# Kernel optimization log

Hardware: AMD Instinct MI355X
Metric: run time of the kernel (lower is better)

## Reference

```python
import jax, jax.numpy as jnp
import numpy as np

T, H, I, SI, E, K = 1024, 2048, 1408, 5632, 8, 4
NORM_TOPK_PROB = False


def setup_inputs() -> dict:
    key = jax.random.key(0)
    ks = jax.random.split(key, 9)
    s = lambda k, shape, fan: (jax.random.normal(k, shape, jnp.float32) * (fan ** -0.5))
    return {
        "hidden_states": jax.random.normal(ks[0], (T, H), jnp.float32),
        "Wg": s(ks[1], (E, H, I), H),   # per-expert gate_proj
        "Wu": s(ks[2], (E, H, I), H),   # per-expert up_proj
        "Wd": s(ks[3], (E, I, H), I),   # per-expert down_proj
        "Wsg": s(ks[4], (H, SI), H),    # shared expert gate_proj
        "Wsu": s(ks[5], (H, SI), H),    # shared expert up_proj
        "Wsd": s(ks[6], (SI, H), SI),   # shared expert down_proj
        "W_router": s(ks[7], (H, E), H),        # self.gate
        "W_shared_gate": s(ks[8], (H, 1), H),   # self.shared_expert_gate
    }


def reference(hidden_states, Wg, Wu, Wd, Wsg, Wsu, Wsd, W_router, W_shared_gate):
    x = hidden_states  # [T, H]
    # shared expert: silu(x Wg) * (x Wu) then down proj (fused_gate_up + matmul)
    shared = (jax.nn.silu(x @ Wsg) * (x @ Wsu)) @ Wsd          # [T, H]
    shared_gate = jax.nn.sigmoid(x @ W_shared_gate)            # [T, 1]
    # router: softmax in float32, then top-k
    probs = jax.nn.softmax((x @ W_router).astype(jnp.float32), axis=-1)  # [T, E]
    top_v, top_i = jax.lax.top_k(probs, K)                     # [T, K]
    if NORM_TOPK_PROB and K > 1:
        top_v = top_v / jnp.sum(top_v, axis=-1, keepdims=True)
    # combine weights: zero for non-routed (expert, token) pairs -> same math
    # as the original gather/expert/scatter(index_add_) loop
    combine = jnp.zeros((T, E), top_v.dtype).at[jnp.arange(T)[:, None], top_i].set(top_v)
    # expert GEMMs (dequantized-GPTQ math): silu(x Wg_e) * (x Wu_e) @ Wd_e
    g = jnp.einsum('th,ehi->eti', x, Wg)                       # [E, T, I]
    u = jnp.einsum('th,ehi->eti', x, Wu)                       # [E, T, I]
    y = jnp.einsum('eti,eih->eth', jax.nn.silu(g) * u, Wd)     # [E, T, H]
    moe = jnp.einsum('eth,te->th', y, combine.astype(x.dtype)) # [T, H]
    scale = 1.0 / (K ** 0.5)
    return (moe + shared_gate * shared) * jnp.asarray(scale, x.dtype)
```

## Files before the change

### kernel.cpp

```cpp
#include <hip/hip_runtime.h>
#include <cstdint>
#include <cstddef>


typedef unsigned short u16;
typedef _Float16 f16;
typedef __attribute__((ext_vector_type(8))) _Float16 half8;
typedef __attribute__((ext_vector_type(4))) float f32x4;

#define GLDS(g, l) __builtin_amdgcn_global_load_lds(                          \
    (const __attribute__((address_space(1))) void*)(g),                       \
    (__attribute__((address_space(3))) void*)(l), 16, 0, 0)

__device__ __forceinline__ float b2f(u16 u){ return __uint_as_float(((uint32_t)u)<<16); }
__device__ __forceinline__ u16 f2b(float f){
  uint32_t x = __float_as_uint(f);
  return (u16)((x + 0x7fffu + ((x>>16)&1u)) >> 16);
}

__global__ __launch_bounds__(64) void detect_kernel(const uint32_t* __restrict__ X,
                                                    int* __restrict__ flag){
  const int lane = threadIdx.x;
  int cnt = 0;
  for (int i = lane; i < 256; i += 64){
    const uint32_t e = (X[i] >> 23) & 0xffu;
    cnt += (e >= 90u && e <= 160u) ? 1 : 0;
  }
#pragma unroll
  for (int off = 32; off > 0; off >>= 1) cnt += __shfl_xor(cnt, off, 64);
  if (lane == 0) *flag = (cnt > 128) ? 1 : 0;
}

template<bool F32>
__device__ void router_conv_body(const void* X, const void* Wr, const void* Wxg,
                                 f16* __restrict__ Xh, float* __restrict__ combine,
                                 float* __restrict__ sgate, float (*red)[9]){
  const int t = blockIdx.x, tid = threadIdx.x, lane = tid&63, wave = tid>>6;
  const int h0 = tid*8;
  float xv[8], gv[8];
  if (F32){
    const float* xp = (const float*)X + (size_t)t*2048 + h0;
    const float4 a = *(const float4*)xp, b = *(const float4*)(xp+4);
    xv[0]=a.x; xv[1]=a.y; xv[2]=a.z; xv[3]=a.w;
    xv[4]=b.x; xv[5]=b.y; xv[6]=b.z; xv[7]=b.w;
    const float* gp = (const float*)Wxg + h0;
    const float4 c = *(const float4*)gp, d = *(const float4*)(gp+4);
    gv[0]=c.x; gv[1]=c.y; gv[2]=c.z; gv[3]=c.w;
    gv[4]=d.x; gv[5]=d.y; gv[6]=d.z; gv[7]=d.w;
  } else {
    union { uint4 v; u16 s[8]; } xr, gr;
    xr.v = *(const uint4*)((const u16*)X + (size_t)t*2048 + h0);
    gr.v = *(const uint4*)((const u16*)Wxg + h0);
#pragma unroll
    for (int q = 0; q < 8; ++q){ xv[q] = b2f(xr.s[q]); gv[q] = b2f(gr.s[q]); }
  }
  half8 h8;
#pragma unroll
  for (int j = 0; j < 8; ++j) h8[j] = (f16)xv[j];
  *(half8*)(Xh + (size_t)t*2048 + h0) = h8;

  float acc[8] = {0,0,0,0,0,0,0,0};
  float ag = 0.f;
#pragma unroll
  for (int jj = 0; jj < 8; ++jj){
    const int h = h0 + jj;
    float w[8];
    if (F32){
      const float* wp = (const float*)Wr + (size_t)h*8;
      const float4 w0 = *(const float4*)wp, w1 = *(const float4*)(wp+4);
      w[0]=w0.x; w[1]=w0.y; w[2]=w0.z; w[3]=w0.w;
      w[4]=w1.x; w[5]=w1.y; w[6]=w1.z; w[7]=w1.w;
    } else {
      union { uint4 v; u16 s[8]; } wv;
      wv.v = *(const uint4*)((const u16*)Wr + (size_t)h*8);
#pragma unroll
      for (int q = 0; q < 8; ++q) w[q] = b2f(wv.s[q]);
    }
#pragma unroll
    for (int e = 0; e < 8; ++e) acc[e] += xv[jj] * w[e];
    ag += xv[jj] * gv[jj];
  }
#pragma unroll
  for (int off = 32; off > 0; off >>= 1){
#pragma unroll
    for (int e = 0; e < 8; ++e) acc[e] += __shfl_xor(acc[e], off, 64);
    ag += __shfl_xor(ag, off, 64);
  }
  if (lane == 0){
#pragma unroll
    for (int e = 0; e < 8; ++e) red[wave][e] = acc[e];
    red[wave][8] = ag;
  }
  __syncthreads();
  if (tid == 0){
    float a[8], g = 0.f;
#pragma unroll
    for (int e = 0; e < 8; ++e) a[e] = red[0][e] + red[1][e] + red[2][e] + red[3][e];
    g = red[0][8] + red[1][8] + red[2][8] + red[3][8];
    float m = a[0];
#pragma unroll
    for (int e = 1; e < 8; ++e) m = fmaxf(m, a[e]);
    float p[8]; float s = 0.f;
#pragma unroll
    for (int e = 0; e < 8; ++e){ p[e] = __expf(a[e]-m); s += p[e]; }
    const float inv = 1.f/s;
#pragma unroll
    for (int e = 0; e < 8; ++e) p[e] *= inv;
#pragma unroll
    for (int e = 0; e < 8; ++e){
      int cnt = 0;
#pragma unroll
      for (int j = 0; j < 8; ++j)
        cnt += (p[j] > p[e]) || (p[j] == p[e] && j < e);
      combine[(size_t)t*8 + e] = (cnt < 4) ? p[e] : 0.f;
    }
    sgate[t] = 1.f/(1.f + __expf(-g));
  }
}
__global__ __launch_bounds__(256) void router_conv(const void* X, const void* Wr, const void* Wxg,
                                                   f16* Xh, float* combine, float* sgate,
                                                   const int* flag){
  __shared__ float red[4][9];
  if (*flag) router_conv_body<true >(X, Wr, Wxg, Xh, combine, sgate, red);
  else       router_conv_body<false>(X, Wr, Wxg, Xh, combine, sgate, red);
}

__device__ void compact256(const float* __restrict__ combine, int* __restrict__ cnt,
                           int* __restrict__ tok, float* __restrict__ cw,
                           int* __restrict__ inv, int* lc){
  const int tid = threadIdx.x;
  if (tid < 8) lc[tid] = 0;
  __syncthreads();
#pragma unroll
  for (int s = 0; s < 4; ++s){
    const int t = s*256 + tid;
    int k = 0;
#pragma unroll
    for (int e = 0; e < 8; ++e){
      const float v = combine[(size_t)t*8 + e];
      if (v > 0.f){
        const int p = atomicAdd(&lc[e], 1);
        tok[e*1024 + p] = t;
        cw [e*1024 + p] = v;
        if (k < 4) inv[t*4 + k] = e*1024 + p;
        ++k;
      }
    }
    for (; k < 4; ++k) inv[t*4 + k] = -1;
  }
  __syncthreads();
#pragma unroll
  for (int e = 0; e < 8; ++e)
    for (int i = tid; i < 1024; i += 256)
      if (i >= lc[e]){ tok[e*1024 + i] = 0; cw[e*1024 + i] = 0.f; }
  if (tid < 8) cnt[tid] = lc[tid];
}

#define TP 72
template<bool F32>
__device__ void tcvt64(const void* S, f16* __restrict__ Dm, int K, int N,
                       size_t soff, int n0, int k0, f16* Tt){
  const int t = threadIdx.x;
  const int kr = t >> 4, nc = (t & 15)*4;
#pragma unroll
  for (int p = 0; p < 4; ++p){
    const int kk = p*16 + kr;
    float v0, v1, v2, v3;
    if (F32){
      const float* Sm = (const float*)S + soff;
      const float4 v = *(const float4*)(Sm + (size_t)(k0+kk)*N + n0 + nc);
      v0=v.x; v1=v.y; v2=v.z; v3=v.w;
    } else {
      const u16* Sm = (const u16*)S + soff;
      union { uint2 u; u16 s[4]; } r;
      r.u = *(const uint2*)(Sm + (size_t)(k0+kk)*N + n0 + nc);
      v0=b2f(r.s[0]); v1=b2f(r.s[1]); v2=b2f(r.s[2]); v3=b2f(r.s[3]);
    }
    Tt[(nc+0)*TP + kk] = (f16)v0;
    Tt[(nc+1)*TP + kk] = (f16)v1;
    Tt[(nc+2)*TP + kk] = (f16)v2;
    Tt[(nc+3)*TP + kk] = (f16)v3;
  }
  __syncthreads();
  const int nr = t >> 3, kc = (t & 7)*8;
#pragma unroll
  for (int p = 0; p < 2; ++p){
    const int n = p*32 + nr;
    const half8 v = *(const half8*)(Tt + n*TP + kc);
    *(half8*)(Dm + (size_t)(n0+n)*K + k0 + kc) = v;
  }
}

__global__ __launch_bounds__(256) void prep_gu(
    const void* Wsg, const void* Wsu, const void* Wg, const void* Wu,
    f16* WsgT, f16* WsuT, f16* WgT, f16* WuT,
    const float* combine, int* cnt, int* tok, float* cw, int* inv,
    const int* flag){
  __shared__ f16 Tt[64*TP];
  int bid = blockIdx.x;
  if (bid == 16896){
    compact256(combine, cnt, tok, cw, inv, (int*)Tt);
    return;
  }
  const void* S; f16* D; int K, N, nx; size_t soff = 0;
  if (bid < 2816){ S = Wsg; D = WsgT; K = 2048; N = 5632; nx = 88; }
  else if (bid < 5632){ bid -= 2816; S = Wsu; D = WsuT; K = 2048; N = 5632; nx = 88; }
  else if (bid < 11264){
    bid -= 5632; const int z = bid/704; bid -= z*704;
    soff = (size_t)z*2048*1408;
    S = Wg; D = WgT + soff; K = 2048; N = 1408; nx = 22;
  } else {
    bid -= 11264; const int z = bid/704; bid -= z*704;
    soff = (size_t)z*2048*1408;
    S = Wu; D = WuT + soff; K = 2048; N = 1408; nx = 22;
  }
  const int n0 = (bid % nx)*64, k0 = (bid / nx)*64;
  if (*flag) tcvt64<true >(S, D, K, N, soff, n0, k0, Tt);
  else       tcvt64<false>(S, D, K, N, soff, n0, k0, Tt);
}

__device__ __forceinline__ void stage_T128(const f16* __restrict__ Row, int ld, int k0, f16* Ls){
  const int tid = threadIdx.x, wave = tid>>6, lane = tid&63;
#pragma unroll
  for (int i = 0; i < 2; ++i){
    const int rbase = i*64 + wave*16;
    const f16* g = Row + (size_t)(rbase + (lane>>2))*ld + (k0 + (lane&3)*8);
    GLDS(g, Ls + rbase*32);
  }
}
__device__ __forceinline__ void stage_T64(const f16* __restrict__ Row, int ld, int k0, f16* Ls){
  const int tid = threadIdx.x, wave = tid>>6, lane = tid&63;
  const int rbase = wave*16;
  const f16* g = Row + (size_t)(rbase + (lane>>2))*ld + (k0 + (lane&3)*8);
  GLDS(g, Ls + rbase*32);
}

__device__ void gu_body_t(
    const f16* __restrict__ Xh, const f16* __restrict__ WsgT, const f16* __restrict__ WsuT,
    const f16* __restrict__ WgT, const f16* __restrict__ WuT,
    f16* __restrict__ A1s, f16* __restrict__ P,
    const float* __restrict__ sgate, const float* __restrict__ cw,
    const int* __restrict__ cnt, const int* __restrict__ tok,
    int bid, f16* As, f16* Bg, f16* Bu)
{
  const int tid = threadIdx.x, lane = tid&63, wave = tid>>6;
  const f16 *BgRow, *BuRow; f16* outp; const float* rs;
  int ldout, m0, n0;
  const f16 *gA0, *gA1;
  if (bid < 704){
    n0 = (bid % 88)*64; m0 = (bid / 88)*128;
    BgRow = WsgT + (size_t)n0*2048; BuRow = WsuT + (size_t)n0*2048;
    outp = A1s; rs = sgate; ldout = 5632;
    const int r0 = m0 + wave*16 + (lane>>2);
    gA0 = Xh + (size_t)r0*2048 + (lane&3)*8;
    gA1 = gA0 + (size_t)64*2048;
  } else {
    bid -= 704;
    const int e = bid / 176, r = bid % 176;
    const int mt = r / 22;
    if (mt*128 >= cnt[e]) return;
    n0 = (r % 22)*64; m0 = mt*128;
    const size_t off = (size_t)e*1408*2048;
    BgRow = WgT + off + (size_t)n0*2048; BuRow = WuT + off + (size_t)n0*2048;
    outp = P + (size_t)e*1024*1408; rs = cw + e*1024; ldout = 1408;
    const int* tp = tok + e*1024 + m0;
    const int t0 = tp[wave*16 + (lane>>2)];
    const int t1 = tp[64 + wave*16 + (lane>>2)];
    gA0 = Xh + (size_t)t0*2048 + (lane&3)*8;
    gA1 = Xh + (size_t)t1*2048 + (lane&3)*8;
  }
  const int wm = wave>>1, wn = wave&1, lr = lane&15, q = lane>>4;

  const f32x4 z4 = {0.f,0.f,0.f,0.f};
  f32x4 ag[4][2], au[4][2];
#pragma unroll
  for (int mi = 0; mi < 4; ++mi)
#pragma unroll
    for (int ni = 0; ni < 2; ++ni){ ag[mi][ni] = z4; au[mi][ni] = z4; }

  for (int k0 = 0; k0 < 2048; k0 += 32){
    __syncthreads();
    GLDS(gA0 + k0, As + wave*512);
    GLDS(gA1 + k0, As + 2048 + wave*512);
    stage_T64(BgRow, 2048, k0, Bg);
    stage_T64(BuRow, 2048, k0, Bu);
    __syncthreads();
    half8 af[4];
#pragma unroll
    for (int mi = 0; mi < 4; ++mi)
      af[mi] = *(const half8*)(As + (wm*64 + mi*16 + lr)*32 + q*8);
#pragma unroll
    for (int ni = 0; ni < 2; ++ni){
      const half8 bfg = *(const half8*)(Bg + (wn*32 + ni*16 + lr)*32 + q*8);
      const half8 bfu = *(const half8*)(Bu + (wn*32 + ni*16 + lr)*32 + q*8);
#pragma unroll
      for (int mi = 0; mi < 4; ++mi){
        ag[mi][ni] = __builtin_amdgcn_mfma_f32_16x16x32_f16(af[mi], bfg, ag[mi][ni], 0, 0, 0);
        au[mi][ni] = __builtin_amdgcn_mfma_f32_16x16x32_f16(af[mi], bfu, au[mi][ni], 0, 0, 0);
      }
    }
  }

  float rsv[4][4];
#pragma unroll
  for (int mi = 0; mi < 4; ++mi)
#pragma unroll
    for (int r = 0; r < 4; ++r)
      rsv[mi][r] = rs[m0 + wm*64 + mi*16 + q*4 + r];
#pragma unroll
  for (int mi = 0; mi < 4; ++mi)
#pragma unroll
    for (int ni = 0; ni < 2; ++ni)
#pragma unroll
      for (int r = 0; r < 4; ++r){
        const int row = m0 + wm*64 + mi*16 + q*4 + r;
        const int col = n0 + wn*32 + ni*16 + lr;
        const float g = ag[mi][ni][r];
        const float v = (g / (1.f + __expf(-g))) * au[mi][ni][r] * rsv[mi][r];
        outp[(size_t)row*ldout + col] = (f16)v;
      }
}

__global__ __launch_bounds__(256) void gu_fused(
    const f16* __restrict__ Xh, const f16* __restrict__ WsgT, const f16* __restrict__ WsuT,
    const f16* __restrict__ WgT, const f16* __restrict__ WuT,
    f16* __restrict__ A1s, f16* __restrict__ P,
    const float* __restrict__ sgate, const float* __restrict__ cw,
    const int* __restrict__ cnt, const int* __restrict__ tok,
    const void* Wd, const void* Wsd, f16* WdT, f16* WsdT, const int* flag)
{
  __shared__ __align__(16) char smbuf[16384];
  const int bid = blockIdx.x;
  const int g = bid/5, r = bid%5;
  if (r == 0){
    f16* As = (f16*)smbuf;
    f16* Bg = (f16*)(smbuf + 8192);
    f16* Bu = (f16*)(smbuf + 12288);
    gu_body_t(Xh, WsgT, WsuT, WgT, WuT, A1s, P, sgate, cw, cnt, tok, g, As, Bg, Bu);
    return;
  }
  int idx = 4*g + (r-1);
  f16* Tt = (f16*)smbuf;
  const void* S; f16* D; int K, N, nx;
  if (idx < 5632){ S = Wd; D = WdT; K = 11264; N = 2048; nx = 32; }
  else { idx -= 5632; S = Wsd; D = WsdT; K = 5632; N = 2048; nx = 32; }
  const int n0 = (idx % nx)*64, k0 = (idx / nx)*64;
  if (*flag) tcvt64<true >(S, D, K, N, 0, n0, k0, Tt);
  else       tcvt64<false>(S, D, K, N, 0, n0, k0, Tt);
}

__global__ __launch_bounds__(256) void down_gemm_t(
    const f16* __restrict__ Pm, const f16* __restrict__ A1s,
    const f16* __restrict__ WdT, const f16* __restrict__ WsdT,
    const int* __restrict__ cnt,
    float* __restrict__ downR, float* __restrict__ shp)
{
  __shared__ f16 As[128*32];
  __shared__ f16 Bs[128*32];
  const int z = blockIdx.z;
  const int m0 = blockIdx.y*128, n0 = blockIdx.x*128;
  const f16 *A, *B; int lda, ldk, KT; float* C;
  if (z < 8){
    if (m0 >= cnt[z]) return;
    A = Pm + (size_t)z*1024*1408 + (size_t)m0*1408; lda = 1408;
    B = WdT + (size_t)z*1408; ldk = 11264; KT = 44;
    C = downR + (size_t)z*1024*2048;
  } else {
    A = A1s + (size_t)(z-8)*2816 + (size_t)m0*5632; lda = 5632;
    B = WsdT + (size_t)(z-8)*2816; ldk = 5632; KT = 88;
    C = shp + (size_t)(z-8)*2097152;
  }
  const f16* Arow = A;
  const f16* Brow = B + (size_t)n0*ldk;
  const int tid = threadIdx.x, lane = tid&63, wave = tid>>6;
  const int wm = wave>>1, wn = wave&1, lr = lane&15, q = lane>>4;

  const f32x4 z4 = {0.f,0.f,0.f,0.f};
  f32x4 acc[4][4];
#pragma unroll
  for (int mi = 0; mi < 4; ++mi)
#pragma unroll
    for (int ni = 0; ni < 4; ++ni) acc[mi][ni] = z4;

  for (int kt = 0; kt < KT; ++kt){
    __syncthreads();
    stage_T128(Arow, lda, kt*32, As);
    stage_T128(Brow, ldk, kt*32, Bs);
    __syncthreads();
    half8 af[4], bf[4];
#pragma unroll
    for (int mi = 0; mi < 4; ++mi)
      af[mi] = *(const half8*)(As + (wm*64 + mi*16 + lr)*32 + q*8);
#pragma unroll
    for (int ni = 0; ni < 4; ++ni)
      bf[ni] = *(const half8*)(Bs + (wn*64 + ni*16 + lr)*32 + q*8);
#pragma unroll
    for (int ni = 0; ni < 4; ++ni)
#pragma unroll
      for (int mi = 0; mi < 4; ++mi)
        acc[mi][ni] = __builtin_amdgcn_mfma_f32_16x16x32_f16(af[mi], bf[ni], acc[mi][ni], 0, 0, 0);
  }
#pragma unroll
  for (int mi = 0; mi < 4; ++mi)
#pragma unroll
    for (int ni = 0; ni < 4; ++ni)
#pragma unroll
      for (int r = 0; r < 4; ++r){
        const int row = m0 + wm*64 + mi*16 + q*4 + r;
        const int col = n0 + wn*64 + ni*16 + lr;
        C[(size_t)row*2048 + col] = acc[mi][ni][r];
      }
}

__global__ __launch_bounds__(256) void final_g(
    const float4* __restrict__ sh0, const float4* __restrict__ sh1,
    const float4* __restrict__ downR, const int* __restrict__ inv,
    void* __restrict__ out, const int* __restrict__ flag){
  const int t = blockIdx.x;
  const int4 iv = *(const int4*)(inv + t*4);
  const int idx[4] = {iv.x, iv.y, iv.z, iv.w};
#pragma unroll
  for (int jj = 0; jj < 2; ++jj){
    const int j = threadIdx.x + jj*256;
    const size_t b = (size_t)t*512 + j;
    const float4 a = sh0[b], c = sh1[b];
    float v0 = a.x + c.x, v1 = a.y + c.y, v2 = a.z + c.z, v3 = a.w + c.w;
#pragma unroll
    for (int k = 0; k < 4; ++k){
      if (idx[k] >= 0){
        const float4 d = downR[(size_t)idx[k]*512 + j];
        v0 += d.x; v1 += d.y; v2 += d.z; v3 += d.w;
      }
    }
    v0 *= 0.5f; v1 *= 0.5f; v2 *= 0.5f; v3 *= 0.5f;
    if (*flag){
      float4 o; o.x=v0; o.y=v1; o.z=v2; o.w=v3;
      ((float4*)out)[b] = o;
    } else {
      uint2 o;
      o.x = (uint32_t)f2b(v0) | ((uint32_t)f2b(v1) << 16);
      o.y = (uint32_t)f2b(v2) | ((uint32_t)f2b(v3) << 16);
      ((uint2*)out)[b] = o;
    }
  }
}

#define LDBT 40
#define ABUF 4096
#define BBUF 2560
struct BR { float v[8]; };
template<bool F32>
__device__ __forceinline__ void loadB(const void* __restrict__ B, size_t ldb, int k0, int n0, BR& r){
  const int t = threadIdx.x, c = t&63, kg = t>>6;
  if (F32){
    const float* p = (const float*)B + (size_t)(k0 + kg*8)*ldb + (n0 + c);
#pragma unroll
    for (int j = 0; j < 8; ++j) r.v[j] = p[(size_t)j*ldb];
  } else {
    const u16* p = (const u16*)B + (size_t)(k0 + kg*8)*ldb + (n0 + c);
#pragma unroll
    for (int j = 0; j < 8; ++j) r.v[j] = b2f(p[(size_t)j*ldb]);
  }
}
__device__ __forceinline__ void storeB(const BR& r, f16* BT){
  const int t = threadIdx.x, c = t&63, kg = t>>6;
  half8 h;
#pragma unroll
  for (int j = 0; j < 8; ++j) h[j] = (f16)r.v[j];
  *(half8*)(BT + c*LDBT + kg*8) = h;
}
template<bool F32>
__device__ void gu_body_r(const f16* __restrict__ Arow, const void* __restrict__ Bgp,
                          const void* __restrict__ Bup, f16* __restrict__ outp,
                          const float* __restrict__ rs, int rs_stride,
                          int ldb, int ldout, int m0, int n0,
                          f16* As, f16* BgT, f16* BuT)
{
  const int tid = threadIdx.x, lane = tid&63, wave = tid>>6;
  const int wm = wave>>1, wn = wave&1, lr = lane&15, q = lane>>4;
  const f32x4 z4 = {0.f,0.f,0.f,0.f};
  f32x4 ag[4][2], au[4][2];
#pragma unroll
  for (int mi = 0; mi < 4; ++mi)
#pragma unroll
    for (int ni = 0; ni < 2; ++ni){ ag[mi][ni] = z4; au[mi][ni] = z4; }
  const int KT = 64;
  BR rg, ru;
  loadB<F32>(Bgp, ldb, 0, n0, rg);
  loadB<F32>(Bup, ldb, 0, n0, ru);
  storeB(rg, BgT); storeB(ru, BuT);
  stage_T128(Arow, 2048, 0, As);
  loadB<F32>(Bgp, ldb, 32, n0, rg);
  loadB<F32>(Bup, ldb, 32, n0, ru);
  __syncthreads();
  for (int kt = 0; kt < KT; ++kt){
    const int cur = kt&1, nxt = cur^1;
    if (kt+1 < KT){
      storeB(rg, BgT + nxt*BBUF);
      storeB(ru, BuT + nxt*BBUF);
      stage_T128(Arow, 2048, (kt+1)*32, As + nxt*ABUF);
    }
    if (kt+2 < KT){
      loadB<F32>(Bgp, ldb, (kt+2)*32, n0, rg);
      loadB<F32>(Bup, ldb, (kt+2)*32, n0, ru);
    }
    const f16* Ac = As + cur*ABUF;
    const f16* Bgc = BgT + cur*BBUF;
    const f16* Buc = BuT + cur*BBUF;
    half8 af[4];
#pragma unroll
    for (int mi = 0; mi < 4; ++mi)
      af[mi] = *(const half8*)(Ac + (wm*64 + mi*16 + lr)*32 + q*8);
#pragma unroll
    for (int ni = 0; ni < 2; ++ni){
      const half8 bfg = *(const half8*)(Bgc + (wn*32 + ni*16 + lr)*LDBT + q*8);
      const half8 bfu = *(const half8*)(Buc + (wn*32 + ni*16 + lr)*LDBT + q*8);
#pragma unroll
      for (int mi = 0; mi < 4; ++mi){
        ag[mi][ni] = __builtin_amdgcn_mfma_f32_16x16x32_f16(af[mi], bfg, ag[mi][ni], 0, 0, 0);
        au[mi][ni] = __builtin_amdgcn_mfma_f32_16x16x32_f16(af[mi], bfu, au[mi][ni], 0, 0, 0);
      }
    }
    __syncthreads();
  }
  float rsv[4][4];
#pragma unroll
  for (int mi = 0; mi < 4; ++mi)
#pragma unroll
    for (int r = 0; r < 4; ++r)
      rsv[mi][r] = rs[(size_t)(m0 + wm*64 + mi*16 + q*4 + r)*rs_stride];
#pragma unroll
  for (int mi = 0; mi < 4; ++mi)
#pragma unroll
    for (int ni = 0; ni < 2; ++ni)
#pragma unroll
      for (int r = 0; r < 4; ++r){
        const int row = m0 + wm*64 + mi*16 + q*4 + r;
        const int col = n0 + wn*32 + ni*16 + lr;
        const float g = ag[mi][ni][r];
        const float v = (g / (1.f + __expf(-g))) * au[mi][ni][r] * rsv[mi][r];
        outp[(size_t)row*ldout + col] = (f16)v;
      }
}
__global__ __launch_bounds__(256) void gu_gemm_r(
    const f16* __restrict__ Xh, const void* Wsg, const void* Wsu,
    const void* Wg, const void* Wu, f16* __restrict__ A1s, f16* __restrict__ P,
    const float* __restrict__ sgate, const float* __restrict__ combine, const int* flag)
{
  __shared__ f16 As[2*ABUF];
  __shared__ f16 BgT[2*BBUF];
  __shared__ f16 BuT[2*BBUF];
  const bool f32v = (*flag != 0);
  int bid = blockIdx.x;
  const void *Bg, *Bu; f16* outp; const float* rs;
  int rs_stride, ldb, ldout, m0, n0;
  if (bid < 704){
    n0 = (bid % 88)*64; m0 = (bid / 88)*128;
    Bg = Wsg; Bu = Wsu; outp = A1s; rs = sgate;
    rs_stride = 1; ldb = 5632; ldout = 5632;
  } else {
    bid -= 704;
    const int e = bid / 176, r = bid % 176;
    n0 = (r % 22)*64; m0 = (r / 22)*128;
    const size_t off = (size_t)e*2048*1408;
    Bg = f32v ? (const void*)((const float*)Wg + off) : (const void*)((const u16*)Wg + off);
    Bu = f32v ? (const void*)((const float*)Wu + off) : (const void*)((const u16*)Wu + off);
    outp = P + (size_t)e*1408; rs = combine + e;
    rs_stride = 8; ldb = 1408; ldout = 11264;
  }
  const f16* Arow = Xh + (size_t)m0*2048;
  if (f32v) gu_body_r<true >(Arow, Bg, Bu, outp, rs, rs_stride, ldb, ldout, m0, n0, As, BgT, BuT);
  else      gu_body_r<false>(Arow, Bg, Bu, outp, rs, rs_stride, ldb, ldout, m0, n0, As, BgT, BuT);
}
template<bool F32>
__device__ void down_body_r(const f16* __restrict__ Arow, int lda, const void* __restrict__ B,
                            float* __restrict__ C, int m0, int n0, f16* As, f16* BT)
{
  const int tid = threadIdx.x, lane = tid&63, wave = tid>>6;
  const int wm = wave>>1, wn = wave&1, lr = lane&15, q = lane>>4;
  const f32x4 z4 = {0.f,0.f,0.f,0.f};
  f32x4 acc[4][2];
#pragma unroll
  for (int mi = 0; mi < 4; ++mi)
#pragma unroll
    for (int ni = 0; ni < 2; ++ni) acc[mi][ni] = z4;
  const int KT = 176;
  BR rb;
  loadB<F32>(B, 2048, 0, n0, rb);
  storeB(rb, BT);
  stage_T128(Arow, lda, 0, As);
  loadB<F32>(B, 2048, 32, n0, rb);
  __syncthreads();
  for (int kt = 0; kt < KT; ++kt){
    const int cur = kt&1, nxt = cur^1;
    if (kt+1 < KT){
      storeB(rb, BT + nxt*BBUF);
      stage_T128(Arow, lda, (kt+1)*32, As + nxt*ABUF);
    }
    if (kt+2 < KT) loadB<F32>(B, 2048, (kt+2)*32, n0, rb);
    const f16* Ac = As + cur*ABUF;
    const f16* Bc = BT + cur*BBUF;
    half8 af[4];
#pragma unroll
    for (int mi = 0; mi < 4; ++mi)
      af[mi] = *(const half8*)(Ac + (wm*64 + mi*16 + lr)*32 + q*8);
#pragma unroll
    for (int ni = 0; ni < 2; ++ni){
      const half8 bf = *(const half8*)(Bc + (wn*32 + ni*16 + lr)*LDBT + q*8);
#pragma unroll
      for (int mi = 0; mi < 4; ++mi)
        acc[mi][ni] = __builtin_amdgcn_mfma_f32_16x16x32_f16(af[mi], bf, acc[mi][ni], 0, 0, 0);
    }
    __syncthreads();
  }
#pragma unroll
  for (int mi = 0; mi < 4; ++mi)
#pragma unroll
    for (int ni = 0; ni < 2; ++ni)
#pragma unroll
      for (int r = 0; r < 4; ++r){
        const int row = m0 + wm*64 + mi*16 + q*4 + r;
        const int col = n0 + wn*32 + ni*16 + lr;
        C[(size_t)row*2048 + col] = acc[mi][ni][r];
      }
}
__global__ __launch_bounds__(256) void down_gemm_r(
    const f16* __restrict__ Pm, const f16* __restrict__ A1s,
    const void* Wd, const void* Wsd,
    float* __restrict__ c0, float* __restrict__ c1, float* __restrict__ c2, const int* flag)
{
  __shared__ f16 As[2*ABUF];
  __shared__ f16 BT[2*BBUF];
  const int z = blockIdx.z;
  const bool f32v = (*flag != 0);
  const f16* A; const void* B; float* C; int lda;
  if (z == 0){ A = Pm; B = Wd; C = c0; lda = 11264; }
  else if (z == 1){
    A = Pm + 5632;
    B = f32v ? (const void*)((const float*)Wd + (size_t)5632*2048)
             : (const void*)((const u16*)Wd + (size_t)5632*2048);
    C = c1; lda = 11264;
  } else { A = A1s; B = Wsd; C = c2; lda = 5632; }
  const int m0 = blockIdx.y*128, n0 = blockIdx.x*64;
  const f16* Arow = A + (size_t)m0*lda;
  if (f32v) down_body_r<true >(Arow, lda, B, C, m0, n0, As, BT);
  else      down_body_r<false>(Arow, lda, B, C, m0, n0, As, BT);
}
__global__ __launch_bounds__(256) void final3(
    const float4* __restrict__ b0, const float4* __restrict__ b1, const float4* __restrict__ b2,
    void* __restrict__ out, const int* flag, int n4){
  const int i = blockIdx.x*256 + threadIdx.x;
  if (i >= n4) return;
  const float4 a = b0[i], b = b1[i], c = b2[i];
  const float v0 = 0.5f*(a.x + b.x + c.x);
  const float v1 = 0.5f*(a.y + b.y + c.y);
  const float v2 = 0.5f*(a.z + b.z + c.z);
  const float v3 = 0.5f*(a.w + b.w + c.w);
  if (*flag){
    float4 o; o.x=v0; o.y=v1; o.z=v2; o.w=v3;
    ((float4*)out)[i] = o;
  } else {
    uint2 o;
    o.x = (uint32_t)f2b(v0) | ((uint32_t)f2b(v1) << 16);
    o.y = (uint32_t)f2b(v2) | ((uint32_t)f2b(v3) << 16);
    ((uint2*)out)[i] = o;
  }
}

extern "C" void kernel_launch(void* const* d_in, const int* in_sizes, int n_in,
                              void* d_out, int out_size, void* d_ws, size_t ws_size,
                              hipStream_t stream)
{
  (void)in_sizes; (void)n_in; (void)out_size;
  const void* x   = d_in[0];
  const void* Wg  = d_in[1];
  const void* Wu  = d_in[2];
  const void* Wd  = d_in[3];
  const void* Wsg = d_in[4];
  const void* Wsu = d_in[5];
  const void* Wsd = d_in[6];
  const void* Wr  = d_in[7];
  const void* Wxg = d_in[8];

  char* ws = (char*)d_ws;
  size_t off = 0;
  auto alloc = [&](size_t bytes)->char*{
    char* p = ws + off; off = (off + bytes + 255) & ~(size_t)255; return p;
  };
  float* combine = (float*)alloc(32768);
  float* sgate   = (float*)alloc(4096);
  int*   flag    = (int*)  alloc(4096);
  int*   cnt     = (int*)  alloc(4096);
  int*   tok     = (int*)  alloc(8*1024*4);
  float* cw      = (float*)alloc(8*1024*4);
  int*   inv     = (int*)  alloc(1024*4*4);
  f16*   Xh      = (f16*)  alloc((size_t)1024*2048*2);
  f16*   A1s     = (f16*)  alloc((size_t)1024*5632*2);
  f16*   P       = (f16*)  alloc((size_t)8*1024*1408*2);
  float* shp     = (float*)alloc((size_t)3*2097152*4);
  float* downR   = (float*)alloc((size_t)8*1024*2048*4);
  f16*   WsgT    = (f16*)  alloc((size_t)5632*2048*2);
  f16*   WsuT    = (f16*)  alloc((size_t)5632*2048*2);
  f16*   WgT     = (f16*)  alloc((size_t)8*1408*2048*2);
  f16*   WuT     = (f16*)  alloc((size_t)8*1408*2048*2);
  f16*   WdT     = (f16*)  alloc((size_t)2048*11264*2);
  f16*   WsdT    = (f16*)  alloc((size_t)2048*5632*2);
  const size_t NEED_FULL = off;

  detect_kernel<<<dim3(1), dim3(64), 0, stream>>>((const uint32_t*)x, flag);
  router_conv<<<dim3(1024), dim3(256), 0, stream>>>(x, Wr, Wxg, Xh, combine, sgate, flag);

  if (ws_size >= NEED_FULL){
    prep_gu<<<dim3(16897), dim3(256), 0, stream>>>(
        Wsg, Wsu, Wg, Wu, WsgT, WsuT, WgT, WuT,
        combine, cnt, tok, cw, inv, flag);
    gu_fused<<<dim3(10560), dim3(256), 0, stream>>>(
        Xh, WsgT, WsuT, WgT, WuT, A1s, P, sgate, cw, cnt, tok,
        Wd, Wsd, WdT, WsdT, flag);
    down_gemm_t<<<dim3(16, 8, 10), dim3(256), 0, stream>>>(P, A1s, WdT, WsdT, cnt, downR, shp);
    final_g<<<dim3(1024), dim3(256), 0, stream>>>(
        (const float4*)shp, (const float4*)(shp + 2097152), (const float4*)downR,
        inv, d_out, flag);
  } else {
    float* b0 = shp;
    float* b1 = shp + 2097152;
    float* b2 = shp + 2*2097152;
    gu_gemm_r<<<dim3(2112), dim3(256), 0, stream>>>(
        Xh, Wsg, Wsu, Wg, Wu, A1s, P, sgate, combine, flag);
    down_gemm_r<<<dim3(32, 8, 3), dim3(256), 0, stream>>>(P, A1s, Wd, Wsd, b0, b1, b2, flag);
    final3<<<dim3(2048), dim3(256), 0, stream>>>(
        (const float4*)b0, (const float4*)b1, (const float4*)b2, d_out, flag, 524288);
  }
}
```

Baseline: 672.0 us.

## Enlarge gate/up GEMM M-tile to 256 with 512-thread blocks

Doubles the block size of the fused gate/up kernel to 8 waves and the M tile to 256 rows, so each staged weight tile is reused across twice as many tokens. Waves split B staging between gate and up weights, and the co-scheduled transpose blocks now each handle two 64x64 tiles. This cuts weight traffic per output. It risks more padding waste on partially filled expert tiles, fewer blocks, and occupancy pressure from 512-thread blocks.

```diff
diff --git a/kernel.cpp b/kernel.cpp
--- a/kernel.cpp
+++ b/kernel.cpp
@@ -159,8 +159,7 @@
 #define TP 72
 template<bool F32>
 __device__ void tcvt64(const void* S, f16* __restrict__ Dm, int K, int N,
-                       size_t soff, int n0, int k0, f16* Tt){
-  const int t = threadIdx.x;
+                       size_t soff, int n0, int k0, f16* Tt, int t){
   const int kr = t >> 4, nc = (t & 15)*4;
 #pragma unroll
   for (int p = 0; p < 4; ++p){
@@ -215,8 +214,8 @@
     S = Wu; D = WuT + soff; K = 2048; N = 1408; nx = 22;
   }
   const int n0 = (bid % nx)*64, k0 = (bid / nx)*64;
-  if (*flag) tcvt64<true >(S, D, K, N, soff, n0, k0, Tt);
-  else       tcvt64<false>(S, D, K, N, soff, n0, k0, Tt);
+  if (*flag) tcvt64<true >(S, D, K, N, soff, n0, k0, Tt, threadIdx.x);
+  else       tcvt64<false>(S, D, K, N, soff, n0, k0, Tt, threadIdx.x);
 }
 
 __device__ __forceinline__ void stage_T128(const f16* __restrict__ Row, int ld, int k0, f16* Ls){
@@ -227,12 +226,6 @@
     const f16* g = Row + (size_t)(rbase + (lane>>2))*ld + (k0 + (lane&3)*8);
     GLDS(g, Ls + rbase*32);
   }
-}
-__device__ __forceinline__ void stage_T64(const f16* __restrict__ Row, int ld, int k0, f16* Ls){
-  const int tid = threadIdx.x, wave = tid>>6, lane = tid&63;
-  const int rbase = wave*16;
-  const f16* g = Row + (size_t)(rbase + (lane>>2))*ld + (k0 + (lane&3)*8);
-  GLDS(g, Ls + rbase*32);
 }
 
 __device__ void gu_body_t(
@@ -247,29 +240,33 @@
   const f16 *BgRow, *BuRow; f16* outp; const float* rs;
   int ldout, m0, n0;
   const f16 *gA0, *gA1;
-  if (bid < 704){
-    n0 = (bid % 88)*64; m0 = (bid / 88)*128;
+  if (bid < 352){
+    n0 = (bid % 88)*64; m0 = (bid / 88)*256;
     BgRow = WsgT + (size_t)n0*2048; BuRow = WsuT + (size_t)n0*2048;
     outp = A1s; rs = sgate; ldout = 5632;
-    const int r0 = m0 + wave*16 + (lane>>2);
+    const int r0 = m0 + wave*32 + (lane>>2);
     gA0 = Xh + (size_t)r0*2048 + (lane&3)*8;
-    gA1 = gA0 + (size_t)64*2048;
+    gA1 = gA0 + (size_t)16*2048;
   } else {
-    bid -= 704;
-    const int e = bid / 176, r = bid % 176;
+    bid -= 352;
+    const int e = bid / 88, r = bid % 88;
     const int mt = r / 22;
-    if (mt*128 >= cnt[e]) return;
-    n0 = (r % 22)*64; m0 = mt*128;
+    if (mt*256 >= cnt[e]) return;
+    n0 = (r % 22)*64; m0 = mt*256;
     const size_t off = (size_t)e*1408*2048;
     BgRow = WgT + off + (size_t)n0*2048; BuRow = WuT + off + (size_t)n0*2048;
     outp = P + (size_t)e*1024*1408; rs = cw + e*1024; ldout = 1408;
     const int* tp = tok + e*1024 + m0;
-    const int t0 = tp[wave*16 + (lane>>2)];
-    const int t1 = tp[64 + wave*16 + (lane>>2)];
+    const int t0 = tp[wave*32 + (lane>>2)];
+    const int t1 = tp[wave*32 + 16 + (lane>>2)];
     gA0 = Xh + (size_t)t0*2048 + (lane&3)*8;
     gA1 = Xh + (size_t)t1*2048 + (lane&3)*8;
   }
   const int wm = wave>>1, wn = wave&1, lr = lane&15, q = lane>>4;
+  const int brbase = (wave & 3)*16;
+  const f16* gB = ((wave < 4) ? BgRow : BuRow)
+                + (size_t)(brbase + (lane>>2))*2048 + (lane&3)*8;
+  f16* LB = ((wave < 4) ? Bg : Bu) + brbase*32;
 
   const f32x4 z4 = {0.f,0.f,0.f,0.f};
   f32x4 ag[4][2], au[4][2];
@@ -280,10 +277,9 @@
 
   for (int k0 = 0; k0 < 2048; k0 += 32){
     __syncthreads();
-    GLDS(gA0 + k0, As + wave*512);
-    GLDS(gA1 + k0, As + 2048 + wave*512);
-    stage_T64(BgRow, 2048, k0, Bg);
-    stage_T64(BuRow, 2048, k0, Bu);
+    GLDS(gA0 + k0, As + (wave*32)*32);
+    GLDS(gA1 + k0, As + (wave*32 + 16)*32);
+    GLDS(gB  + k0, LB);
     __syncthreads();
     half8 af[4];
 #pragma unroll
@@ -321,7 +317,7 @@
       }
 }
 
-__global__ __launch_bounds__(256) void gu_fused(
+__global__ __launch_bounds__(512) void gu_fused(
     const f16* __restrict__ Xh, const f16* __restrict__ WsgT, const f16* __restrict__ WsuT,
     const f16* __restrict__ WgT, const f16* __restrict__ WuT,
     f16* __restrict__ A1s, f16* __restrict__ P,
@@ -329,24 +325,26 @@
     const int* __restrict__ cnt, const int* __restrict__ tok,
     const void* Wd, const void* Wsd, f16* WdT, f16* WsdT, const int* flag)
 {
-  __shared__ __align__(16) char smbuf[16384];
+  __shared__ __align__(16) char smbuf[24576];
   const int bid = blockIdx.x;
   const int g = bid/5, r = bid%5;
   if (r == 0){
     f16* As = (f16*)smbuf;
-    f16* Bg = (f16*)(smbuf + 8192);
-    f16* Bu = (f16*)(smbuf + 12288);
+    f16* Bg = (f16*)(smbuf + 16384);
+    f16* Bu = (f16*)(smbuf + 20480);
     gu_body_t(Xh, WsgT, WsuT, WgT, WuT, A1s, P, sgate, cw, cnt, tok, g, As, Bg, Bu);
     return;
   }
-  int idx = 4*g + (r-1);
-  f16* Tt = (f16*)smbuf;
+  const int sub = threadIdx.x >> 8;
+  int idx = (4*g + (r-1))*2 + sub;
+  f16* Tt = (f16*)(smbuf + sub*9216);
   const void* S; f16* D; int K, N, nx;
   if (idx < 5632){ S = Wd; D = WdT; K = 11264; N = 2048; nx = 32; }
   else { idx -= 5632; S = Wsd; D = WsdT; K = 5632; N = 2048; nx = 32; }
   const int n0 = (idx % nx)*64, k0 = (idx / nx)*64;
-  if (*flag) tcvt64<true >(S, D, K, N, 0, n0, k0, Tt);
-  else       tcvt64<false>(S, D, K, N, 0, n0, k0, Tt);
+  const int t = threadIdx.x & 255;
+  if (*flag) tcvt64<true >(S, D, K, N, 0, n0, k0, Tt, t);
+  else       tcvt64<false>(S, D, K, N, 0, n0, k0, Tt, t);
 }
 
 __global__ __launch_bounds__(256) void down_gemm_t(
@@ -714,7 +712,7 @@
     prep_gu<<<dim3(16897), dim3(256), 0, stream>>>(
         Wsg, Wsu, Wg, Wu, WsgT, WsuT, WgT, WuT,
         combine, cnt, tok, cw, inv, flag);
-    gu_fused<<<dim3(10560), dim3(256), 0, stream>>>(
+    gu_fused<<<dim3(5280), dim3(512), 0, stream>>>(
         Xh, WsgT, WsuT, WgT, WuT, A1s, P, sgate, cw, cnt, tok,
         Wd, Wsd, WdT, WsdT, flag);
     down_gemm_t<<<dim3(16, 8, 10), dim3(256), 0, stream>>>(P, A1s, WdT, WsdT, cnt, downR, shp);
```

Result: no change. 675.4 us (+0.5%).
